# Kernel tuning notes

Measured on AMD Instinct MI355X. Metric: run time of the kernel, lower is better.

The kernel has to match this reference:

```python
import jax, jax.numpy as jnp
import numpy as np

B, T, D, H = 4, 2048, 1024, 16
S = D // H  # head dim

def setup_inputs() -> dict:
    key = jax.random.key(0)
    kx, kq, ku, kb = jax.random.split(key, 4)
    x = jax.random.normal(kx, (B, T, D), dtype=jnp.float32)
    # torch nn.Linear weights: (out, in); y = x @ W.T
    Wq = jax.random.normal(kq, (D, D), dtype=jnp.float32) * (1.0 / np.sqrt(D))
    Wu = jax.random.normal(ku, (D, D), dtype=jnp.float32) * (1.0 / np.sqrt(D))
    bu = jax.random.normal(kb, (D,), dtype=jnp.float32) * 0.01
    return {"x": x, "Wq": Wq, "Wu": Wu, "bu": bu}

def reference(x, Wq, Wu, bu):
    b, t, k = x.shape
    h, s = H, S
    # Bug in original module replicated: Q, K, V all use to_queries.
    q = x @ Wq.T  # (b,t,k)
    qh = q.reshape(b, t, h, s).transpose(0, 2, 1, 3)  # (b,h,t,s)
    scores = jnp.einsum('bhts,bhus->bhtu', qh, qh) / jnp.sqrt(jnp.asarray(s, x.dtype))
    w = jax.nn.softmax(scores, axis=-1)  # (b,h,t,t)
    out = jnp.einsum('bhtu,bhus->bhts', w, qh)  # (b,h,t,s)
    out = out.transpose(0, 2, 1, 3).reshape(b, t, k)  # merge heads
    return out @ Wu.T + bu
```

## Files before the change

### kernel.cpp

```cpp
#include <hip/hip_runtime.h>

#define B_ 4
#define T_ 2048
#define D_ 1024
#define H_ 16
#define S_ 64

typedef __attribute__((ext_vector_type(8))) short bf16x8;
typedef __attribute__((ext_vector_type(16))) float f32x16;
typedef unsigned int uint;

__device__ __forceinline__ short f2bf(float f) {
    union { float f; uint u; } v; v.f = f;
    uint r = v.u + 0x7fffu + ((v.u >> 16) & 1u);
    return (short)(r >> 16);
}

__device__ __forceinline__ void gld16(const short* g, short* l) {
    __builtin_amdgcn_global_load_lds((const __attribute__((address_space(1))) void*)g,
                                     (__attribute__((address_space(3))) void*)l, 16, 0, 0);
}

__global__ __launch_bounds__(256) void cvt3(const float* __restrict__ x,
                                            const float* __restrict__ wq,
                                            const float* __restrict__ wu,
                                            short* __restrict__ xb,
                                            short* __restrict__ wqb,
                                            short* __restrict__ wub) {
    const int NX = B_ * T_ * D_ / 8;
    const int NW = D_ * D_ / 8;
    int i = blockIdx.x * 256 + threadIdx.x;
    const float* src; short* dst; int off;
    if (i < NX)            { src = x;  dst = xb;  off = i; }
    else if (i < NX + NW)  { src = wq; dst = wqb; off = i - NX; }
    else                   { src = wu; dst = wub; off = i - NX - NW; }
    float4 a = *(const float4*)(src + (size_t)off * 8);
    float4 b = *(const float4*)(src + (size_t)off * 8 + 4);
    short o[8] = {f2bf(a.x), f2bf(a.y), f2bf(a.z), f2bf(a.w),
                  f2bf(b.x), f2bf(b.y), f2bf(b.z), f2bf(b.w)};
    *(bf16x8*)(dst + (size_t)off * 8) = *(bf16x8*)o;
}

#define STAGE_G(t, bi) do {                                                       \
        int kk_ = (t) << 5;                                                       \
        gld16(Ap + (size_t)lane * K        + kk_ + wv * 8, &As[bi][(wv * 128) * 8]);      \
        gld16(Ap + (size_t)(64 + lane) * K + kk_ + wv * 8, &As[bi][(wv * 128 + 64) * 8]); \
        gld16(Bp + (size_t)lane * K        + kk_ + wv * 8, &Bs[bi][(wv * 128) * 8]);      \
        gld16(Bp + (size_t)(64 + lane) * K + kk_ + wv * 8, &Bs[bi][(wv * 128 + 64) * 8]); \
    } while (0)

template <bool OUT_BF16>
__global__ __launch_bounds__(256, 2) void gemm_bt(const short* __restrict__ A,
                                                  const short* __restrict__ Bt,
                                                  const float* __restrict__ bias,
                                                  void* __restrict__ Cv,
                                                  int M, int N, int K) {
    __shared__ short As[3][4096];
    __shared__ short Bs[3][4096];
    const int tid  = threadIdx.x;
    const int lane = tid & 63;
    const int wv   = tid >> 6;
    const int wm   = wv >> 1, wn = wv & 1;
    const int h32  = lane >> 5;

    int bx = blockIdx.x, by = blockIdx.y;
    {
        const int nbx = gridDim.x, nby = gridDim.y;
        if ((nby & 7) == 0) {
            int f = blockIdx.x + nbx * blockIdx.y;
            int xcd = f & 7, slot = f >> 3;
            bx = slot % nbx;
            by = xcd * (nby >> 3) + slot / nbx;
        }
    }
    const int m0 = by * 128, n0 = bx * 128;
    const short* Ap = A + (size_t)m0 * K;
    const short* Bp = Bt + (size_t)n0 * K;

    f32x16 acc[2][2];
    #pragma unroll
    for (int i = 0; i < 2; ++i)
        #pragma unroll
        for (int j = 0; j < 2; ++j)
            #pragma unroll
            for (int r = 0; r < 16; ++r) acc[i][j][r] = 0.f;

    const int nt = K >> 5;
    STAGE_G(0, 0);
    STAGE_G(1, 1);

    int bi = 0, bs = 2;
    for (int t = 0; t < nt; ++t) {
        if (t + 1 < nt) asm volatile("s_waitcnt vmcnt(4)" ::: "memory");
        else            asm volatile("s_waitcnt vmcnt(0)" ::: "memory");
        __builtin_amdgcn_s_barrier();
        asm volatile("" ::: "memory");

        if (t + 2 < nt) STAGE_G(t + 2, bs);

        const short* Ab = As[bi];
        const short* Bb = Bs[bi];
        #pragma unroll
        for (int ks2 = 0; ks2 < 2; ++ks2) {
            const int kk8 = ks2 * 2 + h32;
            bf16x8 af0  = *(bf16x8*)&Ab[(kk8 * 128 + wm * 64 + (lane & 31)) * 8];
            bf16x8 af1  = *(bf16x8*)&Ab[(kk8 * 128 + wm * 64 + 32 + (lane & 31)) * 8];
            bf16x8 bfr0 = *(bf16x8*)&Bb[(kk8 * 128 + wn * 64 + (lane & 31)) * 8];
            bf16x8 bfr1 = *(bf16x8*)&Bb[(kk8 * 128 + wn * 64 + 32 + (lane & 31)) * 8];
            acc[0][0] = __builtin_amdgcn_mfma_f32_32x32x16_bf16(af0, bfr0, acc[0][0], 0, 0, 0);
            acc[0][1] = __builtin_amdgcn_mfma_f32_32x32x16_bf16(af0, bfr1, acc[0][1], 0, 0, 0);
            acc[1][0] = __builtin_amdgcn_mfma_f32_32x32x16_bf16(af1, bfr0, acc[1][0], 0, 0, 0);
            acc[1][1] = __builtin_amdgcn_mfma_f32_32x32x16_bf16(af1, bfr1, acc[1][1], 0, 0, 0);
        }

        bi = (bi == 2) ? 0 : bi + 1;
        bs = (bs == 2) ? 0 : bs + 1;
    }

    #pragma unroll
    for (int mt = 0; mt < 2; ++mt) {
        #pragma unroll
        for (int nt2 = 0; nt2 < 2; ++nt2) {
            const int rbase = m0 + wm * 64 + mt * 32;
            const int col   = n0 + wn * 64 + nt2 * 32 + (lane & 31);
            float bv = 0.f;
            if (!OUT_BF16 && bias) bv = bias[col];
            #pragma unroll
            for (int r = 0; r < 16; ++r) {
                int row = rbase + (r & 3) + 8 * (r >> 2) + 4 * h32;
                if constexpr (OUT_BF16)
                    ((short*)Cv)[(size_t)row * N + col] = f2bf(acc[mt][nt2][r]);
                else
                    ((float*)Cv)[(size_t)row * N + col] = acc[mt][nt2][r] + bv;
            }
        }
    }
}

__global__ __launch_bounds__(256, 3) void attn_mfma(const short* __restrict__ q,
                                                    short* __restrict__ o) {
    __shared__ short smem[16384];
    const int tid  = threadIdx.x;
    const int lane = tid & 63;
    const int wv   = tid >> 6;
    const int h32  = lane >> 5;
    const int b  = blockIdx.y >> 4;
    const int hh = blockIdx.y & 15;
    const int t0 = blockIdx.x * 128;
    const short* qb = q + (size_t)b * (T_ * D_) + hh * S_;

    const int c8  = tid & 7;
    const int uu0 = tid >> 3;
    const int uu1 = uu0 + 32;
    const int u_0 = (uu0 & 0x33) | ((uu0 & 4) << 1) | ((uu0 & 8) >> 1);
    const int u_1 = (uu1 & 0x33) | ((uu1 & 4) << 1) | ((uu1 & 8) >> 1);
    const int kfo0 = (c8 * 64 + (u_0 ^ c8)) * 8;
    const int kfo1 = (c8 * 64 + (u_1 ^ c8)) * 8;
    const int kto0 = 4096 + (u_0 >> 4) * 1024 + ((u_0 >> 2) & 1) * 512 + (c8 >> 2) * 8
                   + ((u_0 & 3) | (((u_0 >> 3) & 1) << 2)) + (c8 & 3) * 16;
    const int kto1 = 4096 + (u_1 >> 4) * 1024 + ((u_1 >> 2) & 1) * 512 + (c8 >> 2) * 8
                   + ((u_1 & 3) | (((u_1 >> 3) & 1) << 2)) + (c8 & 3) * 16;
    const short* g0 = qb + (size_t)u_0 * D_ + c8 * 8;
    const short* g1 = qb + (size_t)u_1 * D_ + c8 * 8;

    bf16x8 st0 = *(const bf16x8*)g0;
    bf16x8 st1 = *(const bf16x8*)g1;
    #pragma unroll
    for (int rep = 0; rep < 4; ++rep) {
        int f = rep * 256 + tid;
        int r = f >> 3, cq = f & 7;
        bf16x8 v = *(const bf16x8*)(qb + (size_t)(t0 + r) * D_ + cq * 8);
        *(bf16x8*)&smem[(cq * 128 + (r ^ cq)) * 8] = v;
    }
    __syncthreads();
    bf16x8 Qreg[4];
    #pragma unroll
    for (int ks = 0; ks < 4; ++ks) {
        int kk8 = 2 * ks + h32;
        Qreg[ks] = *(bf16x8*)&smem[(kk8 * 128 + ((wv * 32 + (lane & 31)) ^ kk8)) * 8];
    }
    __syncthreads();
    *(bf16x8*)&smem[kfo0] = st0;
    *(bf16x8*)&smem[kfo1] = st1;
    #pragma unroll
    for (int ds = 0; ds < 8; ++ds) {
        smem[kto0 + ds * 64] = st0[ds];
        smem[kto1 + ds * 64] = st1[ds];
    }
    st0 = *(const bf16x8*)(g0 + (size_t)64 * D_);
    st1 = *(const bf16x8*)(g1 + (size_t)64 * D_);

    f32x16 accO0, accO1;
    #pragma unroll
    for (int i = 0; i < 16; ++i) { accO0[i] = 0.f; accO1[i] = 0.f; }
    float lsp0 = 0.f, lsp1 = 0.f;
    const int prow16 = ((((lane & 7) << 2) | ((lane >> 3) & 3)) * 16) + h32 * 512;
    const float SCL = 0.18033688f;

    int rb = 0;
    for (int u0 = 0; u0 < T_; u0 += 64) {
        __syncthreads();
        const int wb = rb ^ 8192;

        f32x16 aS0, aS1;
        #pragma unroll
        for (int i = 0; i < 16; ++i) { aS0[i] = 0.f; aS1[i] = 0.f; }
        __builtin_amdgcn_s_setprio(1);
        #pragma unroll
        for (int ks = 0; ks < 4; ++ks) {
            int kk8 = 2 * ks + h32;
            bf16x8 k0 = *(bf16x8*)&smem[rb + (kk8 * 64 + ((lane & 31) ^ kk8)) * 8];
            bf16x8 k1 = *(bf16x8*)&smem[rb + (kk8 * 64 + ((32 + (lane & 31)) ^ kk8)) * 8];
            aS0 = __builtin_amdgcn_mfma_f32_32x32x16_bf16(k0, Qreg[ks], aS0, 0, 0, 0);
            aS1 = __builtin_amdgcn_mfma_f32_32x32x16_bf16(k1, Qreg[ks], aS1, 0, 0, 0);
        }
        __builtin_amdgcn_s_setprio(0);

        *(bf16x8*)&smem[wb + kfo0] = st0;
        *(bf16x8*)&smem[wb + kfo1] = st1;
        #pragma unroll
        for (int ds = 0; ds < 8; ++ds) {
            smem[wb + kto0 + ds * 64] = st0[ds];
            smem[wb + kto1 + ds * 64] = st1[ds];
        }
        int un = u0 + 128; if (un >= T_) un = 0;
        st0 = *(const bf16x8*)(g0 + (size_t)un * D_);
        st1 = *(const bf16x8*)(g1 + (size_t)un * D_);

        bf16x8 af[4];
        #pragma unroll
        for (int tt = 0; tt < 2; ++tt) {
            const f32x16& a = tt ? aS1 : aS0;
            float p[16];
            #pragma unroll
            for (int r = 0; r < 16; r += 2) {
                p[r]     = __builtin_amdgcn_exp2f(a[r] * SCL);
                p[r + 1] = __builtin_amdgcn_exp2f(a[r + 1] * SCL);
                lsp0 += p[r];
                lsp1 += p[r + 1];
            }
            #pragma unroll
            for (int sub = 0; sub < 2; ++sub) {
                union { uint u[4]; bf16x8 v; } cv;
                #pragma unroll
                for (int dd = 0; dd < 4; ++dd)
                    cv.u[dd] = __builtin_amdgcn_perm(
                        __float_as_uint(p[sub * 8 + 2 * dd + 1]),
                        __float_as_uint(p[sub * 8 + 2 * dd]), 0x07060302u);
                af[tt * 2 + sub] = cv.v;
            }
        }

        __builtin_amdgcn_s_setprio(1);
        #pragma unroll
        for (int c = 0; c < 4; ++c) {
            bf16x8 v0 = *(bf16x8*)&smem[rb + 4096 + c * 1024 + prow16 + 0];
            bf16x8 v1 = *(bf16x8*)&smem[rb + 4096 + c * 1024 + prow16 + 8];
            accO0 = __builtin_amdgcn_mfma_f32_32x32x16_bf16(af[c], v0, accO0, 0, 0, 0);
            accO1 = __builtin_amdgcn_mfma_f32_32x32x16_bf16(af[c], v1, accO1, 0, 0, 0);
        }
        __builtin_amdgcn_s_setprio(0);
        rb = wb;
    }

    float lsp = lsp0 + lsp1;
    float dsum = lsp + __shfl_xor(lsp, 32);
    short* ob = o + (size_t)b * (T_ * D_) + hh * S_;
    #pragma unroll
    for (int r = 0; r < 16; ++r) {
        int rt = (r & 3) + 8 * (r >> 2) + 4 * h32;
        float inv = 1.00390625f / __shfl(dsum, rt);
        size_t t = (size_t)(t0 + wv * 32 + rt);
        ob[t * D_ + (lane & 31)]      = f2bf(accO0[r] * inv);
        ob[t * D_ + 32 + (lane & 31)] = f2bf(accO1[r] * inv);
    }
}

extern "C" void kernel_launch(void* const* d_in, const int* in_sizes, int n_in,
                              void* d_out, int out_size, void* d_ws, size_t ws_size,
                              hipStream_t stream) {
    const float* x  = (const float*)d_in[0];
    const float* Wq = (const float*)d_in[1];
    const float* Wu = (const float*)d_in[2];
    const float* bu = (const float*)d_in[3];
    float* out  = (float*)d_out;
    short* qbuf = (short*)d_out;
    short* xb   = (short*)((char*)d_out + 16777216);
    short* attn = (short*)d_ws;
    short* wqb  = (short*)((char*)d_ws + 16777216);
    short* wub  = (short*)((char*)d_ws + 18874368);

    const int M = B_ * T_;
    dim3 blk(256);
    dim3 gg(D_ / 128, M / 128);
    hipLaunchKernelGGL(cvt3, dim3(5120), blk, 0, stream, x, Wq, Wu, xb, wqb, wub);
    hipLaunchKernelGGL((gemm_bt<true>), gg, blk, 0, stream,
                       xb, wqb, (const float*)nullptr, (void*)qbuf, M, D_, D_);
    hipLaunchKernelGGL(attn_mfma, dim3(T_ / 128, B_ * H_), blk, 0, stream, qbuf, attn);
    hipLaunchKernelGGL((gemm_bt<false>), gg, blk, 0, stream,
                       attn, wub, bu, (void*)out, M, D_, D_);
}
```

Measured before the change: 245.2 us.

## Restructure GEMM to 8 waves with BK=64 double-buffered LDS tiles

The projection GEMM moves from 256-thread blocks with a triple-buffered BK=32 pipeline to 512-thread blocks with a double-buffered BK=64 pipeline. Each of the 8 waves now computes a 32x64 sub-tile with two accumulators instead of a 64x64 tile with four. The aim is more resident waves for latency hiding and half as many barriers per K. In exchange, prefetch depth drops to one stage with a full vmcnt(0) wait each iteration, and each block uses 64KB of LDS, which limits how many blocks fit per CU.

Measured after the change: 249.5 us. About the same (+1.7%).

```diff
diff --git a/kernel.cpp b/kernel.cpp
--- a/kernel.cpp
+++ b/kernel.cpp
@@ -42,7 +42,7 @@
 }
 
 #define STAGE_G(t, bi) do {                                                       \
-        int kk_ = (t) << 5;                                                       \
+        int kk_ = (t) << 6;                                                       \
         gld16(Ap + (size_t)lane * K        + kk_ + wv * 8, &As[bi][(wv * 128) * 8]);      \
         gld16(Ap + (size_t)(64 + lane) * K + kk_ + wv * 8, &As[bi][(wv * 128 + 64) * 8]); \
         gld16(Bp + (size_t)lane * K        + kk_ + wv * 8, &Bs[bi][(wv * 128) * 8]);      \
@@ -50,17 +50,18 @@
     } while (0)
 
 template <bool OUT_BF16>
-__global__ __launch_bounds__(256, 2) void gemm_bt(const short* __restrict__ A,
+__global__ __launch_bounds__(512, 4) void gemm_bt(const short* __restrict__ A,
                                                   const short* __restrict__ Bt,
                                                   const float* __restrict__ bias,
                                                   void* __restrict__ Cv,
                                                   int M, int N, int K) {
-    __shared__ short As[3][4096];
-    __shared__ short Bs[3][4096];
+    __shared__ short As[2][8192];
+    __shared__ short Bs[2][8192];
     const int tid  = threadIdx.x;
     const int lane = tid & 63;
     const int wv   = tid >> 6;
-    const int wm   = wv >> 1, wn = wv & 1;
+    const int wm   = wv >> 1;
+    const int wn   = wv & 1;
     const int h32  = lane >> 5;
 
     int bx = blockIdx.x, by = blockIdx.y;
@@ -77,62 +78,49 @@
     const short* Ap = A + (size_t)m0 * K;
     const short* Bp = Bt + (size_t)n0 * K;
 
-    f32x16 acc[2][2];
+    f32x16 acc[2];
     #pragma unroll
     for (int i = 0; i < 2; ++i)
         #pragma unroll
-        for (int j = 0; j < 2; ++j)
-            #pragma unroll
-            for (int r = 0; r < 16; ++r) acc[i][j][r] = 0.f;
-
-    const int nt = K >> 5;
+        for (int r = 0; r < 16; ++r) acc[i][r] = 0.f;
+
+    const int nt = K >> 6;
     STAGE_G(0, 0);
-    STAGE_G(1, 1);
-
-    int bi = 0, bs = 2;
+
     for (int t = 0; t < nt; ++t) {
-        if (t + 1 < nt) asm volatile("s_waitcnt vmcnt(4)" ::: "memory");
-        else            asm volatile("s_waitcnt vmcnt(0)" ::: "memory");
+        const int cur = t & 1;
+        asm volatile("s_waitcnt vmcnt(0)" ::: "memory");
         __builtin_amdgcn_s_barrier();
         asm volatile("" ::: "memory");
 
-        if (t + 2 < nt) STAGE_G(t + 2, bs);
-
-        const short* Ab = As[bi];
-        const short* Bb = Bs[bi];
-        #pragma unroll
-        for (int ks2 = 0; ks2 < 2; ++ks2) {
-            const int kk8 = ks2 * 2 + h32;
-            bf16x8 af0  = *(bf16x8*)&Ab[(kk8 * 128 + wm * 64 + (lane & 31)) * 8];
-            bf16x8 af1  = *(bf16x8*)&Ab[(kk8 * 128 + wm * 64 + 32 + (lane & 31)) * 8];
-            bf16x8 bfr0 = *(bf16x8*)&Bb[(kk8 * 128 + wn * 64 + (lane & 31)) * 8];
-            bf16x8 bfr1 = *(bf16x8*)&Bb[(kk8 * 128 + wn * 64 + 32 + (lane & 31)) * 8];
-            acc[0][0] = __builtin_amdgcn_mfma_f32_32x32x16_bf16(af0, bfr0, acc[0][0], 0, 0, 0);
-            acc[0][1] = __builtin_amdgcn_mfma_f32_32x32x16_bf16(af0, bfr1, acc[0][1], 0, 0, 0);
-            acc[1][0] = __builtin_amdgcn_mfma_f32_32x32x16_bf16(af1, bfr0, acc[1][0], 0, 0, 0);
-            acc[1][1] = __builtin_amdgcn_mfma_f32_32x32x16_bf16(af1, bfr1, acc[1][1], 0, 0, 0);
-        }
-
-        bi = (bi == 2) ? 0 : bi + 1;
-        bs = (bs == 2) ? 0 : bs + 1;
-    }
-
-    #pragma unroll
-    for (int mt = 0; mt < 2; ++mt) {
-        #pragma unroll
-        for (int nt2 = 0; nt2 < 2; ++nt2) {
-            const int rbase = m0 + wm * 64 + mt * 32;
-            const int col   = n0 + wn * 64 + nt2 * 32 + (lane & 31);
-            float bv = 0.f;
-            if (!OUT_BF16 && bias) bv = bias[col];
-            #pragma unroll
-            for (int r = 0; r < 16; ++r) {
-                int row = rbase + (r & 3) + 8 * (r >> 2) + 4 * h32;
-                if constexpr (OUT_BF16)
-                    ((short*)Cv)[(size_t)row * N + col] = f2bf(acc[mt][nt2][r]);
-                else
-                    ((float*)Cv)[(size_t)row * N + col] = acc[mt][nt2][r] + bv;
-            }
+        if (t + 1 < nt) STAGE_G(t + 1, cur ^ 1);
+
+        const short* Ab = As[cur];
+        const short* Bb = Bs[cur];
+        #pragma unroll
+        for (int ks = 0; ks < 4; ++ks) {
+            const int kk8 = ks * 2 + h32;
+            bf16x8 af = *(bf16x8*)&Ab[(kk8 * 128 + wm * 32 + (lane & 31)) * 8];
+            bf16x8 b0 = *(bf16x8*)&Bb[(kk8 * 128 + wn * 64 + (lane & 31)) * 8];
+            bf16x8 b1 = *(bf16x8*)&Bb[(kk8 * 128 + wn * 64 + 32 + (lane & 31)) * 8];
+            acc[0] = __builtin_amdgcn_mfma_f32_32x32x16_bf16(af, b0, acc[0], 0, 0, 0);
+            acc[1] = __builtin_amdgcn_mfma_f32_32x32x16_bf16(af, b1, acc[1], 0, 0, 0);
+        }
+    }
+
+    const int rbase = m0 + wm * 32;
+    #pragma unroll
+    for (int nt2 = 0; nt2 < 2; ++nt2) {
+        const int col = n0 + wn * 64 + nt2 * 32 + (lane & 31);
+        float bv = 0.f;
+        if (!OUT_BF16 && bias) bv = bias[col];
+        #pragma unroll
+        for (int r = 0; r < 16; ++r) {
+            int row = rbase + (r & 3) + 8 * (r >> 2) + 4 * h32;
+            if constexpr (OUT_BF16)
+                ((short*)Cv)[(size_t)row * N + col] = f2bf(acc[nt2][r]);
+            else
+                ((float*)Cv)[(size_t)row * N + col] = acc[nt2][r] + bv;
         }
     }
 }
@@ -291,12 +279,11 @@
     short* wub  = (short*)((char*)d_ws + 18874368);
 
     const int M = B_ * T_;
-    dim3 blk(256);
     dim3 gg(D_ / 128, M / 128);
-    hipLaunchKernelGGL(cvt3, dim3(5120), blk, 0, stream, x, Wq, Wu, xb, wqb, wub);
-    hipLaunchKernelGGL((gemm_bt<true>), gg, blk, 0, stream,
+    hipLaunchKernelGGL(cvt3, dim3(5120), dim3(256), 0, stream, x, Wq, Wu, xb, wqb, wub);
+    hipLaunchKernelGGL((gemm_bt<true>), gg, dim3(512), 0, stream,
                        xb, wqb, (const float*)nullptr, (void*)qbuf, M, D_, D_);
-    hipLaunchKernelGGL(attn_mfma, dim3(T_ / 128, B_ * H_), blk, 0, stream, qbuf, attn);
-    hipLaunchKernelGGL((gemm_bt<false>), gg, blk, 0, stream,
+    hipLaunchKernelGGL(attn_mfma, dim3(T_ / 128, B_ * H_), dim3(256), 0, stream, qbuf, attn);
+    hipLaunchKernelGGL((gemm_bt<false>), gg, dim3(512), 0, stream,
                        attn, wub, bu, (void*)out, M, D_, D_);
 }
```
